# Kernel tuning notes

Hardware: AMD Instinct MI355X
Metric: run time of the kernel (lower is better)

## Reference

```python
import jax, jax.numpy as jnp
import numpy as np

DIM = 1024
INTER = 512
E = 32            # n_routed_experts
TOPK = 4          # n_activated_experts
GROUPS = 8        # n_expert_groups
TOPK_GROUPS = 4
SHARED_INTER = 2 * INTER  # n_shared_experts * moe_inter_dim
ROUTE_SCALE = 1.0
B, S = 8, 4096


def setup_inputs() -> dict:
    key = jax.random.key(0)
    ks = jax.random.split(key, 16)
    def xav(k, shape):
        fan_in, fan_out = shape[-2], shape[-1]
        lim = np.sqrt(6.0 / (fan_in + fan_out))
        return jax.random.uniform(k, shape, jnp.float32, -lim, lim)
    return {
        "x": jax.random.normal(ks[0], (B, S, DIM), jnp.float32),
        "gw": xav(ks[1], (DIM, E)),
        "gb": jnp.zeros((E,), jnp.float32),
        "w1": xav(ks[2], (E, DIM, INTER)),
        "b1": jnp.zeros((E, INTER), jnp.float32),
        "w3": xav(ks[3], (E, DIM, INTER)),
        "b3": jnp.zeros((E, INTER), jnp.float32),
        "w2": xav(ks[4], (E, INTER, DIM)),
        "b2": jnp.zeros((E, DIM), jnp.float32),
        "sw1": xav(ks[5], (DIM, SHARED_INTER)),
        "sb1": jnp.zeros((SHARED_INTER,), jnp.float32),
        "sw3": xav(ks[6], (DIM, SHARED_INTER)),
        "sb3": jnp.zeros((SHARED_INTER,), jnp.float32),
        "sw2": xav(ks[7], (SHARED_INTER, DIM)),
        "sb2": jnp.zeros((DIM,), jnp.float32),
    }


def _gate(xf, gw, gb):
    # scores: softmax over routed experts in fp32 (score_func='softmax')
    T = xf.shape[0]
    scores = jax.nn.softmax((xf @ gw + gb).astype(jnp.float32), axis=-1)  # [T, E]
    original_scores = scores
    # group-masked routing (n_expert_groups > 1)
    scores_g = scores.reshape(T, GROUPS, E // GROUPS)                     # [T, G, E/G]
    group_scores = jnp.sum(jax.lax.top_k(scores_g, 2)[0], axis=-1)        # [T, G]
    gidx = jax.lax.top_k(group_scores, TOPK_GROUPS)[1]                    # [T, topk_groups]
    keep = jnp.zeros((T, GROUPS), bool).at[jnp.arange(T)[:, None], gidx].set(True)
    masked = jnp.where(keep[:, :, None], scores_g, -jnp.inf).reshape(T, E)
    indices = jax.lax.top_k(masked, TOPK)[1]                              # [T, topk]
    weights = jnp.take_along_axis(original_scores, indices, axis=1) * ROUTE_SCALE
    return weights.astype(xf.dtype), indices


def reference(x, gw, gb, w1, b1, w3, b3, w2, b2, sw1, sb1, sw3, sb3, sw2, sb2):
    shape = x.shape
    xf = x.reshape(-1, DIM)                                               # [T, dim]
    T = xf.shape[0]
    weights, indices = _gate(xf, gw, gb)
    # dense combine weights [T, E]: w_e(t) = routing weight if expert e chosen for t else 0
    cw = jnp.zeros((T, E), xf.dtype).at[jnp.arange(T)[:, None], indices].add(weights)
    # scan over experts: y += w_e * SwiGLU_e(x). Zero weight -> zero contribution,
    # identical math to the masked dispatch/scatter-add in the torch code.
    def body(y, p):
        w1e, b1e, w3e, b3e, w2e, b2e, we = p
        h = jax.nn.silu(xf @ w1e + b1e) * (xf @ w3e + b3e)                # [T, inter]
        return y + we[:, None] * (h @ w2e + b2e), None
    y0 = jnp.zeros_like(xf)
    y, _ = jax.lax.scan(body, y0, (w1, b1, w3, b3, w2, b2, cw.T))
    # shared experts MLP (SwiGLU)
    z = (jax.nn.silu(xf @ sw1 + sb1) * (xf @ sw3 + sb3)) @ sw2 + sb2
    return (y + z).reshape(shape)
```

## Files before the change

kernel.cpp:

```cpp
#include <hip/hip_runtime.h>
#include <stdint.h>

#define DIM_    1024
#define INTER_  512

typedef short bf16x4 __attribute__((ext_vector_type(4)));
typedef short bf16x8 __attribute__((ext_vector_type(8)));
typedef float f32x4  __attribute__((ext_vector_type(4)));

__device__ __forceinline__ unsigned short f2bf(float f) {
  union { float f; unsigned u; } v; v.f = f;
  return (unsigned short)((v.u + 0x7FFFu + ((v.u >> 16) & 1u)) >> 16);
}
__device__ __forceinline__ unsigned f2bf2(float a, float b) {
  union { float f; unsigned u; } va, vb; va.f = a; vb.f = b;
  unsigned ra = (va.u + 0x7FFFu + ((va.u >> 16) & 1u)) >> 16;
  unsigned rb = (vb.u + 0x7FFFu + ((vb.u >> 16) & 1u)) >> 16;
  return ra | (rb << 16);
}
__device__ __forceinline__ float bfhi(unsigned u) {
  union { unsigned u; float f; } v; v.u = u & 0xffff0000u; return v.f;
}
__device__ __forceinline__ float bflo(unsigned u) {
  union { unsigned u; float f; } v; v.u = u << 16; return v.f;
}

__device__ __forceinline__ void gl16(const void* g, void* l) {
  __builtin_amdgcn_global_load_lds(
      (const __attribute__((address_space(1))) unsigned int*)g,
      (__attribute__((address_space(3))) unsigned int*)l, 16, 0, 0);
}

#define BARX() do { asm volatile("" ::: "memory"); \
                    __builtin_amdgcn_s_barrier();  \
                    asm volatile("" ::: "memory"); } while (0)

__global__ __launch_bounds__(256) void gate_kernel(
    const float* __restrict__ x, const float* __restrict__ gw,
    const float* __restrict__ gb, int* __restrict__ idx, float* __restrict__ wts,
    unsigned short* __restrict__ xb) {
  __shared__ double s_sc[4][32];
  __shared__ double s_gs[4][8];
  const int wid = threadIdx.x >> 6, lane = threadIdx.x & 63;
  const int t = blockIdx.x * 4 + wid;
  {
    const float* xrow = x + (size_t)t * DIM_ + lane * 16;
    unsigned short* xbrow = xb + (size_t)t * DIM_ + lane * 16;
    float4 f0 = *(const float4*)(xrow);
    float4 f1 = *(const float4*)(xrow + 4);
    float4 f2v = *(const float4*)(xrow + 8);
    float4 f3v = *(const float4*)(xrow + 12);
    uint4 o0, o1;
    o0.x = f2bf2(f0.x, f0.y);  o0.y = f2bf2(f0.z, f0.w);
    o0.z = f2bf2(f1.x, f1.y);  o0.w = f2bf2(f1.z, f1.w);
    o1.x = f2bf2(f2v.x, f2v.y); o1.y = f2bf2(f2v.z, f2v.w);
    o1.z = f2bf2(f3v.x, f3v.y); o1.w = f2bf2(f3v.z, f3v.w);
    *(uint4*)(xbrow) = o0;
    *(uint4*)(xbrow + 8) = o1;
  }
  const int e = lane & 31, half = lane >> 5;
  const float* xr  = x  + (size_t)t * DIM_ + half * 512;
  const float* gwp = gw + (size_t)half * 512 * 32 + e;
  double a0 = 0, a1 = 0, a2 = 0, a3 = 0;
  for (int k = 0; k < 512; k += 4) {
    float4 xv = *(const float4*)(xr + k);
    a0 += (double)xv.x * (double)gwp[(k + 0) * 32];
    a1 += (double)xv.y * (double)gwp[(k + 1) * 32];
    a2 += (double)xv.z * (double)gwp[(k + 2) * 32];
    a3 += (double)xv.w * (double)gwp[(k + 3) * 32];
  }
  double lg = (a0 + a1) + (a2 + a3);
  lg += __shfl_xor(lg, 32);
  lg += (double)gb[e];
  double m = lg;
  #pragma unroll
  for (int d = 1; d < 32; d <<= 1) m = fmax(m, __shfl_xor(m, d));
  double ex = exp(lg - m);
  double ssum = ex;
  #pragma unroll
  for (int d = 1; d < 32; d <<= 1) ssum += __shfl_xor(ssum, d);
  double sc = ex / ssum;
  double p  = __shfl_xor(sc, 1);
  double m1 = fmax(sc, p), n1 = fmin(sc, p);
  double m2 = __shfl_xor(m1, 2), n2 = __shfl_xor(n1, 2);
  double gs = (m1 >= m2) ? (m1 + fmax(n1, m2)) : (m2 + fmax(n2, m1));
  if (lane < 32) {
    s_sc[wid][e] = sc;
    if ((e & 3) == 0) s_gs[wid][e >> 2] = gs;
  }
  __syncthreads();
  if (lane == 0) {
    unsigned kmask = 0;
    for (int it = 0; it < 4; ++it) {
      int bg = 0; double bv = -1.0;
      for (int g = 0; g < 8; ++g)
        if (!((kmask >> g) & 1u) && s_gs[wid][g] > bv) { bv = s_gs[wid][g]; bg = g; }
      kmask |= 1u << bg;
    }
    unsigned umask = 0;
    for (int slot = 0; slot < 4; ++slot) {
      int be = 0; double bv = -1.0;
      for (int ee = 0; ee < 32; ++ee)
        if (((kmask >> (ee >> 2)) & 1u) && !((umask >> ee) & 1u) && s_sc[wid][ee] > bv) {
          bv = s_sc[wid][ee]; be = ee;
        }
      umask |= 1u << be;
      idx[t * 4 + slot] = be;
      wts[t * 4 + slot] = (float)bv;
    }
  }
}

__global__ __launch_bounds__(256) void count_kernel(const int* __restrict__ idx,
                                                    int* __restrict__ meta) {
  __shared__ int h[32];
  int tid = threadIdx.x;
  if (tid < 32) h[tid] = 0;
  __syncthreads();
  atomicAdd(&h[idx[blockIdx.x * 256 + tid]], 1);
  __syncthreads();
  if (tid < 32 && h[tid]) atomicAdd(&meta[tid], h[tid]);
}

__global__ void scan_kernel(int* __restrict__ meta) {
  int lane = threadIdx.x & 63;
  if (lane < 32) {
    int c = meta[lane];
    int pre = c;
    #pragma unroll
    for (int d = 1; d < 32; d <<= 1) { int t = __shfl_up(pre, d); if (lane >= d) pre += t; }
    int excl = pre - c;
    meta[64 + lane] = excl;
    meta[32 + lane] = excl;
    int nt = (c + 255) >> 8;
    int ntp = nt;
    #pragma unroll
    for (int d = 1; d < 32; d <<= 1) { int t = __shfl_up(ntp, d); if (lane >= d) ntp += t; }
    int ntExcl = ntp - nt;
    for (int k = 0; k < nt; ++k) { meta[128 + ntExcl + k] = lane; meta[1184 + ntExcl + k] = k << 8; }
    if (lane == 31) { meta[96] = excl + c; meta[97] = ntExcl + nt; }
  }
}

__global__ __launch_bounds__(256) void scatter_kernel(
    const int* __restrict__ idx, int* __restrict__ meta,
    int* __restrict__ tok, int* __restrict__ inv) {
  int i = blockIdx.x * 256 + threadIdx.x;
  int lane = threadIdx.x & 63;
  int e = idx[i];
  unsigned long long m = ~0ull;
  #pragma unroll
  for (int b = 0; b < 5; ++b) {
    unsigned long long vote = __ballot((e >> b) & 1);
    m &= ((e >> b) & 1) ? vote : ~vote;
  }
  int leader = __ffsll((long long)m) - 1;
  int rank = __popcll(m & ((1ull << lane) - 1));
  int base = 0;
  if (lane == leader) base = atomicAdd(&meta[32 + e], (int)__popcll(m));
  base = __shfl(base, leader);
  int p = base + rank;
  tok[p] = i >> 2;
  inv[i] = p;
}

__global__ __launch_bounds__(256) void repack_kernel(
    const float* __restrict__ src, unsigned short* __restrict__ dst,
    int K, int N, int tilesPerMat) {
  const int w = blockIdx.x * 4 + (threadIdx.x >> 6);
  const int j = threadIdx.x & 63;
  const int e = w / tilesPerMat, rem = w % tilesPerMat;
  const int kSteps = K >> 5;
  const int nt = rem / kSteps, kq = rem % kSteps;
  const float* s = src + (size_t)e * K * N + (size_t)(kq * 32) * N + nt * 64 + j;
  float v[32];
  #pragma unroll
  for (int kk = 0; kk < 32; ++kk) v[kk] = s[(size_t)kk * N];
  char* d = (char*)dst + (size_t)w * 4096 + j * 64;
  const int sz = (j & 3) ^ ((j >> 2) & 3);
  #pragma unroll
  for (int q = 0; q < 4; ++q) {
    int o = (q ^ sz) * 8;
    uint4 tv;
    tv.x = f2bf2(v[o + 0], v[o + 1]);
    tv.y = f2bf2(v[o + 2], v[o + 3]);
    tv.z = f2bf2(v[o + 4], v[o + 5]);
    tv.w = f2bf2(v[o + 6], v[o + 7]);
    *(uint4*)(d + q * 16) = tv;
  }
}

__global__ __launch_bounds__(256) void repack13_kernel(
    const float* __restrict__ src1, const float* __restrict__ src3,
    unsigned short* __restrict__ dst, int K, int N, int jtTiles) {
  const int w = blockIdx.x * 4 + (threadIdx.x >> 6);
  const int j = threadIdx.x & 63;
  const int kSteps = K >> 5;
  const int tpm = jtTiles * kSteps;
  const int e = w / tpm, rem = w % tpm;
  const int jt = rem / kSteps, kq = rem % kSteps;
  const int jg = jt * 64 + j;
  const int c = ((jg >> 5) << 4) + (jg & 15);
  const float* s = (((jg >> 4) & 1) ? src3 : src1)
                 + (size_t)e * K * N + (size_t)(kq * 32) * N + c;
  float v[32];
  #pragma unroll
  for (int kk = 0; kk < 32; ++kk) v[kk] = s[(size_t)kk * N];
  char* d = (char*)dst + (size_t)w * 4096 + j * 64;
  const int sz = (j & 3) ^ ((j >> 2) & 3);
  #pragma unroll
  for (int q = 0; q < 4; ++q) {
    int o = (q ^ sz) * 8;
    uint4 tv;
    tv.x = f2bf2(v[o + 0], v[o + 1]);
    tv.y = f2bf2(v[o + 2], v[o + 3]);
    tv.z = f2bf2(v[o + 4], v[o + 5]);
    tv.w = f2bf2(v[o + 6], v[o + 7]);
    *(uint4*)(d + q * 16) = tv;
  }
}


#define G8_PRE()                                                              \
  const int tid = threadIdx.x, lane = tid & 63, wave = tid >> 6;              \
  const int wm = wave >> 2, wn = wave & 3;                                    \
  const int f = lane & 15, g = lane >> 4;                                     \
  const int wud = wave >> 2, wlo = wave & 3;                                  \
  const int row_in = wlo * 16 + (lane >> 2);                                  \
  const int szr = (row_in & 3) ^ ((row_in >> 2) & 3);                         \
  const int qs = (((lane & 3) ^ szr) << 4);                                   \
  const int btile_off = wlo * 1024 + lane * 16;                               \
  const int wv1k = wave * 1024;                                               \
  const int awb = wm * 8192;                                                  \
  const int wn4 = wn * 4096;                                                  \
  int aoff[4];                                                                \
  _Pragma("unroll")                                                           \
  for (int ii = 0; ii < 4; ++ii) {                                            \
    int u16 = ii * 16 + f;                                                    \
    aoff[ii] = u16 * 64 + ((g ^ ((u16 & 3) ^ ((u16 >> 2) & 3))) << 4);        \
  }                                                                           \
  f32x4 acc[8][4];                                                            \
  const f32x4 zz = {0.f, 0.f, 0.f, 0.f};                                      \
  _Pragma("unroll")                                                           \
  for (int mi = 0; mi < 8; ++mi)                                              \
    _Pragma("unroll")                                                         \
    for (int ni = 0; ni < 4; ++ni) acc[mi][ni] = zz;

#define G8_PH(p, UMAXv)                                                       \
  {                                                                           \
    const char* sb_ = lds + ((p) >> 1) * 32768;                               \
    const char* ab_ = sb_ + awb + ((p) & 1) * 4096;                           \
    const char* bb_ = sb_ + 16384 + wn4;                                      \
    bf16x8 af_[4], bv_[4];                                                    \
    _Pragma("unroll")                                                         \
    for (int mi = 0; mi < 4; ++mi) af_[mi] = *(const bf16x8*)(ab_ + aoff[mi]);\
    _Pragma("unroll")                                                         \
    for (int ni = 0; ni < 4; ++ni) bv_[ni] = *(const bf16x8*)(bb_ + aoff[ni]);\
    int u_ = I4 + 3 + ((p) >> 1);                                             \
    if (u_ >= (UMAXv)) u_ = (UMAXv) - 1;                                      \
    char* td_ = lds + (((((p) >> 1) + 3) & 3) * 32768);                       \
    if ((p) & 1) {                                                            \
      gl16(pB0 + (size_t)u_ * 4096, td_ + 16384 + wv1k);                      \
      gl16(pB1 + (size_t)u_ * 4096, td_ + 24576 + wv1k);                      \
    } else {                                                                  \
      gl16(pA0 + u_ * 64, td_ + wv1k);                                        \
      gl16(pA1 + u_ * 64, td_ + 8192 + wv1k);                                 \
    }                                                                         \
    BARX();                                                                   \
    __builtin_amdgcn_s_setprio(1);                                            \
    _Pragma("unroll")                                                         \
    for (int ni = 0; ni < 4; ++ni)                                            \
      _Pragma("unroll")                                                       \
      for (int mi = 0; mi < 4; ++mi)                                          \
        acc[((p) & 1) * 4 + mi][ni] = __builtin_amdgcn_mfma_f32_16x16x32_bf16(\
            af_[mi], bv_[ni], acc[((p) & 1) * 4 + mi][ni], 0, 0, 0);          \
    __builtin_amdgcn_s_setprio(0);                                            \
    if ((p) & 1) asm volatile("s_waitcnt vmcnt(8)" ::: "memory");             \
    BARX();                                                                   \
  }

#define G8_BODY(UMAXv)                                                        \
  _Pragma("unroll")                                                           \
  for (int uu = 0; uu < 3; ++uu) {                                            \
    gl16(pA0 + uu * 64, lds + uu * 32768 + wv1k);                             \
    gl16(pA1 + uu * 64, lds + uu * 32768 + 8192 + wv1k);                      \
    gl16(pB0 + (size_t)uu * 4096, lds + uu * 32768 + 16384 + wv1k);           \
    gl16(pB1 + (size_t)uu * 4096, lds + uu * 32768 + 24576 + wv1k);           \
  }                                                                           \
  asm volatile("s_waitcnt vmcnt(8)" ::: "memory");                            \
  BARX();                                                                     \
  for (int I = 0; I < (UMAXv) / 4; ++I) {                                     \
    const int I4 = I * 4;                                                     \
    G8_PH(0, UMAXv); G8_PH(1, UMAXv); G8_PH(2, UMAXv); G8_PH(3, UMAXv);       \
    G8_PH(4, UMAXv); G8_PH(5, UMAXv); G8_PH(6, UMAXv); G8_PH(7, UMAXv);       \
  }

__global__ __launch_bounds__(512, 2) void s1_kernel(
    const unsigned short* __restrict__ xb, const unsigned short* __restrict__ w13,
    const float* __restrict__ sb1, const float* __restrict__ sb3,
    unsigned short* __restrict__ Hs) {
  __shared__ char lds[131072];
  const int m0 = blockIdx.y * 256;
  G8_PRE();
  const char* pA0 = (const char*)xb + (size_t)(m0 + wud * 64 + row_in) * 2048 + qs;
  const char* pA1 = pA0 + (size_t)128 * 2048;
  const char* pB0 = (const char*)w13 + ((size_t)(blockIdx.x * 4 + wud) * 32) * 4096 + btile_off;
  const char* pB1 = (const char*)w13 + ((size_t)(blockIdx.x * 4 + 2 + wud) * 32) * 4096 + btile_off;
  G8_BODY(32);
  const int colb = blockIdx.x * 128;
  #pragma unroll
  for (int p2 = 0; p2 < 2; ++p2) {
    int c = colb + wn * 32 + p2 * 16 + f;
    float bb1 = sb1[c], bb3 = sb3[c];
    #pragma unroll
    for (int m8 = 0; m8 < 8; ++m8) {
      int row = m0 + wm * 128 + (m8 >> 2) * 64 + (m8 & 3) * 16 + g * 4;
      #pragma unroll
      for (int r = 0; r < 4; ++r) {
        float v1 = acc[m8][2 * p2][r] + bb1;
        float v3 = acc[m8][2 * p2 + 1][r] + bb3;
        float h = (v1 / (1.f + __expf(-v1))) * v3;
        Hs[(size_t)(row + r) * 1024 + c] = f2bf(h);
      }
    }
  }
}

__global__ __launch_bounds__(512, 2) void s2_kernel(
    const unsigned short* __restrict__ Hs, const unsigned short* __restrict__ b2i,
    const float* __restrict__ sb2, float* __restrict__ out) {
  __shared__ char lds[131072];
  const int m0 = blockIdx.y * 256;
  G8_PRE();
  const char* pA0 = (const char*)Hs + (size_t)(m0 + wud * 64 + row_in) * 2048 + qs;
  const char* pA1 = pA0 + (size_t)128 * 2048;
  const char* pB0 = (const char*)b2i + ((size_t)(blockIdx.x * 4 + wud) * 32) * 4096 + btile_off;
  const char* pB1 = (const char*)b2i + ((size_t)(blockIdx.x * 4 + 2 + wud) * 32) * 4096 + btile_off;
  G8_BODY(32);
  #pragma unroll
  for (int ni = 0; ni < 4; ++ni) {
    int c = blockIdx.x * 256 + wn * 64 + ni * 16 + f;
    float bb = sb2[c];
    #pragma unroll
    for (int m8 = 0; m8 < 8; ++m8) {
      int row = m0 + wm * 128 + (m8 >> 2) * 64 + (m8 & 3) * 16 + g * 4;
      #pragma unroll
      for (int r = 0; r < 4; ++r)
        out[(size_t)(row + r) * 1024 + c] = acc[m8][ni][r] + bb;
    }
  }
}

__global__ __launch_bounds__(512, 2) void g1_kernel(
    const unsigned short* __restrict__ xb, const unsigned short* __restrict__ w13,
    const float* __restrict__ b1, const float* __restrict__ b3,
    const int* __restrict__ tok, const int* __restrict__ meta,
    unsigned short* __restrict__ H) {
  __shared__ char lds[131072];
  if ((int)blockIdx.y >= meta[97]) return;
  const int e = meta[128 + blockIdx.y], m0 = meta[1184 + blockIdx.y];
  const int off_e = meta[64 + e], nrem = meta[e] - m0;
  G8_PRE();
  const int r0a = wud * 64 + row_in;
  const int ix0 = off_e + m0 + ((r0a < nrem) ? r0a : 0);
  const int ix1 = off_e + m0 + ((r0a + 128 < nrem) ? r0a + 128 : 0);
  const char* pA0 = (const char*)xb + (size_t)tok[ix0] * 2048 + qs;
  const char* pA1 = (const char*)xb + (size_t)tok[ix1] * 2048 + qs;
  const char* pB0 = (const char*)w13 + ((size_t)(e * 16 + blockIdx.x * 4 + wud) * 32) * 4096 + btile_off;
  const char* pB1 = (const char*)w13 + ((size_t)(e * 16 + blockIdx.x * 4 + 2 + wud) * 32) * 4096 + btile_off;
  G8_BODY(32);
  const int colb = blockIdx.x * 128;
  #pragma unroll
  for (int p2 = 0; p2 < 2; ++p2) {
    int c = colb + wn * 32 + p2 * 16 + f;
    float bb1 = b1[e * 512 + c], bb3 = b3[e * 512 + c];
    #pragma unroll
    for (int m8 = 0; m8 < 8; ++m8) {
      int row = wm * 128 + (m8 >> 2) * 64 + (m8 & 3) * 16 + g * 4;
      #pragma unroll
      for (int r = 0; r < 4; ++r) {
        if (row + r < nrem) {
          float v1 = acc[m8][2 * p2][r] + bb1;
          float v3 = acc[m8][2 * p2 + 1][r] + bb3;
          float h = (v1 / (1.f + __expf(-v1))) * v3;
          H[(size_t)(off_e + m0 + row + r) * 512 + c] = f2bf(h);
        }
      }
    }
  }
}

__global__ __launch_bounds__(512, 2) void g2_kernel(
    const unsigned short* __restrict__ H, const unsigned short* __restrict__ w2i,
    const float* __restrict__ b2, const int* __restrict__ meta,
    unsigned short* __restrict__ Y, int cbase) {
  __shared__ char lds[131072];
  if ((int)blockIdx.y >= meta[97]) return;
  const int e = meta[128 + blockIdx.y], m0 = meta[1184 + blockIdx.y];
  const int off_e = meta[64 + e], nrem = meta[e] - m0;
  G8_PRE();
  const int r0a = wud * 64 + row_in;
  const int ix0 = off_e + m0 + ((r0a < nrem) ? r0a : 0);
  const int ix1 = off_e + m0 + ((r0a + 128 < nrem) ? r0a + 128 : 0);
  const char* pA0 = (const char*)H + (size_t)ix0 * 1024 + qs;
  const char* pA1 = (const char*)H + (size_t)ix1 * 1024 + qs;
  const int nt0 = (cbase >> 6) + blockIdx.x * 4;
  const char* pB0 = (const char*)w2i + ((size_t)(e * 16 + nt0 + wud) * 16) * 4096 + btile_off;
  const char* pB1 = (const char*)w2i + ((size_t)(e * 16 + nt0 + 2 + wud) * 16) * 4096 + btile_off;
  G8_BODY(16);
  #pragma unroll
  for (int ni = 0; ni < 4; ++ni) {
    int ycol = blockIdx.x * 256 + wn * 64 + ni * 16 + f;
    float bb = b2[e * 1024 + cbase + ycol];
    #pragma unroll
    for (int m8 = 0; m8 < 8; ++m8) {
      int row = wm * 128 + (m8 >> 2) * 64 + (m8 & 3) * 16 + g * 4;
      #pragma unroll
      for (int r = 0; r < 4; ++r) {
        if (row + r < nrem)
          Y[(size_t)(off_e + m0 + row + r) * 512 + ycol] = f2bf(acc[m8][ni][r] + bb);
      }
    }
  }
}

__global__ __launch_bounds__(256) void combine_kernel(
    const unsigned short* __restrict__ Y, const int* __restrict__ inv,
    const float* __restrict__ wts, float* __restrict__ out, int cbase) {
  int t = blockIdx.x * 2 + (threadIdx.x >> 7);
  int c = (threadIdx.x & 127) * 4;
  int4 iv = *(const int4*)(inv + t * 4);
  float4 wv = *(const float4*)(wts + t * 4);
  float* op = out + (size_t)t * 1024 + cbase + c;
  float4 o = *(float4*)op;
  uint2 u;
  u = *(const uint2*)(Y + (size_t)iv.x * 512 + c);
  o.x += wv.x * bflo(u.x); o.y += wv.x * bfhi(u.x);
  o.z += wv.x * bflo(u.y); o.w += wv.x * bfhi(u.y);
  u = *(const uint2*)(Y + (size_t)iv.y * 512 + c);
  o.x += wv.y * bflo(u.x); o.y += wv.y * bfhi(u.x);
  o.z += wv.y * bflo(u.y); o.w += wv.y * bfhi(u.y);
  u = *(const uint2*)(Y + (size_t)iv.z * 512 + c);
  o.x += wv.z * bflo(u.x); o.y += wv.z * bfhi(u.x);
  o.z += wv.z * bflo(u.y); o.w += wv.z * bfhi(u.y);
  u = *(const uint2*)(Y + (size_t)iv.w * 512 + c);
  o.x += wv.w * bflo(u.x); o.y += wv.w * bfhi(u.x);
  o.z += wv.w * bflo(u.y); o.w += wv.w * bfhi(u.y);
  *(float4*)op = o;
}

extern "C" void kernel_launch(void* const* d_in, const int* in_sizes, int n_in,
                              void* d_out, int out_size, void* d_ws, size_t ws_size,
                              hipStream_t stream) {
  const float* x   = (const float*)d_in[0];
  const float* gw  = (const float*)d_in[1];
  const float* gb  = (const float*)d_in[2];
  const float* w1  = (const float*)d_in[3];
  const float* b1  = (const float*)d_in[4];
  const float* w3  = (const float*)d_in[5];
  const float* b3  = (const float*)d_in[6];
  const float* w2  = (const float*)d_in[7];
  const float* b2  = (const float*)d_in[8];
  const float* sw1 = (const float*)d_in[9];
  const float* sb1 = (const float*)d_in[10];
  const float* sw3 = (const float*)d_in[11];
  const float* sb3 = (const float*)d_in[12];
  const float* sw2 = (const float*)d_in[13];
  const float* sb2 = (const float*)d_in[14];
  float* out = (float*)d_out;
  char* ws = (char*)d_ws;

  const size_t OFF_XB   = 134217728;
  const size_t OFF_W13I = 201326592;
  const size_t OFF_W2I  = 268435456;
  const size_t OFF_S13I = 301989888;
  const size_t OFF_SW2I = 306184192;
  const size_t OFF_IDX  = 308281344;
  const size_t OFF_WTS  = 308805632;
  const size_t OFF_TOK  = 309329920;
  const size_t OFF_INV  = 309854208;
  const size_t OFF_META = 310378496;
  if (ws_size < OFF_META + 8960) return;

  unsigned short* H    = (unsigned short*)ws;
  unsigned short* xb   = (unsigned short*)(ws + OFF_XB);
  unsigned short* Yb   = (unsigned short*)(ws + OFF_XB);
  unsigned short* w13i = (unsigned short*)(ws + OFF_W13I);
  unsigned short* w2i  = (unsigned short*)(ws + OFF_W2I);
  unsigned short* s13i = (unsigned short*)(ws + OFF_S13I);
  unsigned short* sw2i = (unsigned short*)(ws + OFF_SW2I);
  int*   idx  = (int*)(ws + OFF_IDX);
  float* wts  = (float*)(ws + OFF_WTS);
  int*   tokl = (int*)(ws + OFF_TOK);
  int*   inv  = (int*)(ws + OFF_INV);
  int*   meta = (int*)(ws + OFF_META);

  hipMemsetAsync(meta, 0, 128, stream);
  gate_kernel<<<dim3(8192), dim3(256), 0, stream>>>(x, gw, gb, idx, wts, xb);
  count_kernel<<<dim3(512), dim3(256), 0, stream>>>(idx, meta);
  scan_kernel<<<dim3(1), dim3(64), 0, stream>>>(meta);
  scatter_kernel<<<dim3(512), dim3(256), 0, stream>>>(idx, meta, tokl, inv);
  repack13_kernel<<<dim3(4096), dim3(256), 0, stream>>>(w1, w3, w13i, 1024, 512, 16);
  repack_kernel<<<dim3(2048), dim3(256), 0, stream>>>(w2, w2i, 512, 1024, 256);
  repack13_kernel<<<dim3(256), dim3(256), 0, stream>>>(sw1, sw3, s13i, 1024, 1024, 32);
  repack_kernel<<<dim3(128), dim3(256), 0, stream>>>(sw2, sw2i, 1024, 1024, 512);
  s1_kernel<<<dim3(8, 128), dim3(512), 0, stream>>>(xb, s13i, sb1, sb3, H);
  s2_kernel<<<dim3(4, 128), dim3(512), 0, stream>>>(H, sw2i, sb2, out);
  g1_kernel<<<dim3(4, 544), dim3(512), 0, stream>>>(xb, w13i, b1, b3, tokl, meta, H);
  g2_kernel<<<dim3(2, 544), dim3(512), 0, stream>>>(H, w2i, b2, meta, Yb, 0);
  combine_kernel<<<dim3(16384), dim3(256), 0, stream>>>(Yb, inv, wts, out, 0);
  g2_kernel<<<dim3(2, 544), dim3(512), 0, stream>>>(H, w2i, b2, meta, Yb, 512);
  combine_kernel<<<dim3(16384), dim3(256), 0, stream>>>(Yb, inv, wts, out, 512);
}
```

Before: 1.641 ms.

## Swizzle GEMM block order across XCDs and reuse B fragments across phases

Flattens the 2D grids of the four grouped/shared GEMM kernels into 1D and remaps block ids so consecutive logical tiles land on the same XCD. The goal is to improve L2 reuse of the shared A/B tiles. It also loads the B LDS fragments only on even phases and keeps them in registers for the following odd phase, cutting redundant LDS reads. This adds register pressure, and the swizzle assumes the block count divides evenly by 8.

```diff
diff --git a/kernel.cpp b/kernel.cpp
--- a/kernel.cpp
+++ b/kernel.cpp
@@ -239,6 +239,7 @@
     int u16 = ii * 16 + f;                                                    \
     aoff[ii] = u16 * 64 + ((g ^ ((u16 & 3) ^ ((u16 >> 2) & 3))) << 4);        \
   }                                                                           \
+  bf16x8 bvp[4];                                                              \
   f32x4 acc[8][4];                                                            \
   const f32x4 zz = {0.f, 0.f, 0.f, 0.f};                                      \
   _Pragma("unroll")                                                           \
@@ -250,12 +251,15 @@
   {                                                                           \
     const char* sb_ = lds + ((p) >> 1) * 32768;                               \
     const char* ab_ = sb_ + awb + ((p) & 1) * 4096;                           \
-    const char* bb_ = sb_ + 16384 + wn4;                                      \
-    bf16x8 af_[4], bv_[4];                                                    \
+    bf16x8 af_[4];                                                            \
     _Pragma("unroll")                                                         \
     for (int mi = 0; mi < 4; ++mi) af_[mi] = *(const bf16x8*)(ab_ + aoff[mi]);\
-    _Pragma("unroll")                                                         \
-    for (int ni = 0; ni < 4; ++ni) bv_[ni] = *(const bf16x8*)(bb_ + aoff[ni]);\
+    if (!((p) & 1)) {                                                         \
+      const char* bb_ = sb_ + 16384 + wn4;                                    \
+      _Pragma("unroll")                                                       \
+      for (int ni = 0; ni < 4; ++ni)                                          \
+        bvp[ni] = *(const bf16x8*)(bb_ + aoff[ni]);                           \
+    }                                                                         \
     int u_ = I4 + 3 + ((p) >> 1);                                             \
     if (u_ >= (UMAXv)) u_ = (UMAXv) - 1;                                      \
     char* td_ = lds + (((((p) >> 1) + 3) & 3) * 32768);                       \
@@ -273,7 +277,7 @@
       _Pragma("unroll")                                                       \
       for (int mi = 0; mi < 4; ++mi)                                          \
         acc[((p) & 1) * 4 + mi][ni] = __builtin_amdgcn_mfma_f32_16x16x32_bf16(\
-            af_[mi], bv_[ni], acc[((p) & 1) * 4 + mi][ni], 0, 0, 0);          \
+            af_[mi], bvp[ni], acc[((p) & 1) * 4 + mi][ni], 0, 0, 0);          \
     __builtin_amdgcn_s_setprio(0);                                            \
     if ((p) & 1) asm volatile("s_waitcnt vmcnt(8)" ::: "memory");             \
     BARX();                                                                   \
@@ -295,19 +299,27 @@
     G8_PH(4, UMAXv); G8_PH(5, UMAXv); G8_PH(6, UMAXv); G8_PH(7, UMAXv);       \
   }
 
+#define XCD_SWZ(GXv)                                                          \
+  const int nb_ = gridDim.x;                                                  \
+  const int b_ = blockIdx.x;                                                  \
+  const int w_ = (b_ & 7) * (nb_ >> 3) + (b_ >> 3);                           \
+  const int bx = w_ % (GXv);                                                  \
+  const int by = w_ / (GXv);
+
 __global__ __launch_bounds__(512, 2) void s1_kernel(
     const unsigned short* __restrict__ xb, const unsigned short* __restrict__ w13,
     const float* __restrict__ sb1, const float* __restrict__ sb3,
     unsigned short* __restrict__ Hs) {
   __shared__ char lds[131072];
-  const int m0 = blockIdx.y * 256;
+  XCD_SWZ(8);
+  const int m0 = by * 256;
   G8_PRE();
   const char* pA0 = (const char*)xb + (size_t)(m0 + wud * 64 + row_in) * 2048 + qs;
   const char* pA1 = pA0 + (size_t)128 * 2048;
-  const char* pB0 = (const char*)w13 + ((size_t)(blockIdx.x * 4 + wud) * 32) * 4096 + btile_off;
-  const char* pB1 = (const char*)w13 + ((size_t)(blockIdx.x * 4 + 2 + wud) * 32) * 4096 + btile_off;
+  const char* pB0 = (const char*)w13 + ((size_t)(bx * 4 + wud) * 32) * 4096 + btile_off;
+  const char* pB1 = (const char*)w13 + ((size_t)(bx * 4 + 2 + wud) * 32) * 4096 + btile_off;
   G8_BODY(32);
-  const int colb = blockIdx.x * 128;
+  const int colb = bx * 128;
   #pragma unroll
   for (int p2 = 0; p2 < 2; ++p2) {
     int c = colb + wn * 32 + p2 * 16 + f;
@@ -330,16 +342,17 @@
     const unsigned short* __restrict__ Hs, const unsigned short* __restrict__ b2i,
     const float* __restrict__ sb2, float* __restrict__ out) {
   __shared__ char lds[131072];
-  const int m0 = blockIdx.y * 256;
+  XCD_SWZ(4);
+  const int m0 = by * 256;
   G8_PRE();
   const char* pA0 = (const char*)Hs + (size_t)(m0 + wud * 64 + row_in) * 2048 + qs;
   const char* pA1 = pA0 + (size_t)128 * 2048;
-  const char* pB0 = (const char*)b2i + ((size_t)(blockIdx.x * 4 + wud) * 32) * 4096 + btile_off;
-  const char* pB1 = (const char*)b2i + ((size_t)(blockIdx.x * 4 + 2 + wud) * 32) * 4096 + btile_off;
+  const char* pB0 = (const char*)b2i + ((size_t)(bx * 4 + wud) * 32) * 4096 + btile_off;
+  const char* pB1 = (const char*)b2i + ((size_t)(bx * 4 + 2 + wud) * 32) * 4096 + btile_off;
   G8_BODY(32);
   #pragma unroll
   for (int ni = 0; ni < 4; ++ni) {
-    int c = blockIdx.x * 256 + wn * 64 + ni * 16 + f;
+    int c = bx * 256 + wn * 64 + ni * 16 + f;
     float bb = sb2[c];
     #pragma unroll
     for (int m8 = 0; m8 < 8; ++m8) {
@@ -357,8 +370,9 @@
     const int* __restrict__ tok, const int* __restrict__ meta,
     unsigned short* __restrict__ H) {
   __shared__ char lds[131072];
-  if ((int)blockIdx.y >= meta[97]) return;
-  const int e = meta[128 + blockIdx.y], m0 = meta[1184 + blockIdx.y];
+  XCD_SWZ(4);
+  if (by >= meta[97]) return;
+  const int e = meta[128 + by], m0 = meta[1184 + by];
   const int off_e = meta[64 + e], nrem = meta[e] - m0;
   G8_PRE();
   const int r0a = wud * 64 + row_in;
@@ -366,10 +380,10 @@
   const int ix1 = off_e + m0 + ((r0a + 128 < nrem) ? r0a + 128 : 0);
   const char* pA0 = (const char*)xb + (size_t)tok[ix0] * 2048 + qs;
   const char* pA1 = (const char*)xb + (size_t)tok[ix1] * 2048 + qs;
-  const char* pB0 = (const char*)w13 + ((size_t)(e * 16 + blockIdx.x * 4 + wud) * 32) * 4096 + btile_off;
-  const char* pB1 = (const char*)w13 + ((size_t)(e * 16 + blockIdx.x * 4 + 2 + wud) * 32) * 4096 + btile_off;
+  const char* pB0 = (const char*)w13 + ((size_t)(e * 16 + bx * 4 + wud) * 32) * 4096 + btile_off;
+  const char* pB1 = (const char*)w13 + ((size_t)(e * 16 + bx * 4 + 2 + wud) * 32) * 4096 + btile_off;
   G8_BODY(32);
-  const int colb = blockIdx.x * 128;
+  const int colb = bx * 128;
   #pragma unroll
   for (int p2 = 0; p2 < 2; ++p2) {
     int c = colb + wn * 32 + p2 * 16 + f;
@@ -395,8 +409,9 @@
     const float* __restrict__ b2, const int* __restrict__ meta,
     unsigned short* __restrict__ Y, int cbase) {
   __shared__ char lds[131072];
-  if ((int)blockIdx.y >= meta[97]) return;
-  const int e = meta[128 + blockIdx.y], m0 = meta[1184 + blockIdx.y];
+  XCD_SWZ(2);
+  if (by >= meta[97]) return;
+  const int e = meta[128 + by], m0 = meta[1184 + by];
   const int off_e = meta[64 + e], nrem = meta[e] - m0;
   G8_PRE();
   const int r0a = wud * 64 + row_in;
@@ -404,13 +419,13 @@
   const int ix1 = off_e + m0 + ((r0a + 128 < nrem) ? r0a + 128 : 0);
   const char* pA0 = (const char*)H + (size_t)ix0 * 1024 + qs;
   const char* pA1 = (const char*)H + (size_t)ix1 * 1024 + qs;
-  const int nt0 = (cbase >> 6) + blockIdx.x * 4;
+  const int nt0 = (cbase >> 6) + bx * 4;
   const char* pB0 = (const char*)w2i + ((size_t)(e * 16 + nt0 + wud) * 16) * 4096 + btile_off;
   const char* pB1 = (const char*)w2i + ((size_t)(e * 16 + nt0 + 2 + wud) * 16) * 4096 + btile_off;
   G8_BODY(16);
   #pragma unroll
   for (int ni = 0; ni < 4; ++ni) {
-    int ycol = blockIdx.x * 256 + wn * 64 + ni * 16 + f;
+    int ycol = bx * 256 + wn * 64 + ni * 16 + f;
     float bb = b2[e * 1024 + cbase + ycol];
     #pragma unroll
     for (int m8 = 0; m8 < 8; ++m8) {
@@ -504,11 +519,11 @@
   repack_kernel<<<dim3(2048), dim3(256), 0, stream>>>(w2, w2i, 512, 1024, 256);
   repack13_kernel<<<dim3(256), dim3(256), 0, stream>>>(sw1, sw3, s13i, 1024, 1024, 32);
   repack_kernel<<<dim3(128), dim3(256), 0, stream>>>(sw2, sw2i, 1024, 1024, 512);
-  s1_kernel<<<dim3(8, 128), dim3(512), 0, stream>>>(xb, s13i, sb1, sb3, H);
-  s2_kernel<<<dim3(4, 128), dim3(512), 0, stream>>>(H, sw2i, sb2, out);
-  g1_kernel<<<dim3(4, 544), dim3(512), 0, stream>>>(xb, w13i, b1, b3, tokl, meta, H);
-  g2_kernel<<<dim3(2, 544), dim3(512), 0, stream>>>(H, w2i, b2, meta, Yb, 0);
+  s1_kernel<<<dim3(1024), dim3(512), 0, stream>>>(xb, s13i, sb1, sb3, H);
+  s2_kernel<<<dim3(512), dim3(512), 0, stream>>>(H, sw2i, sb2, out);
+  g1_kernel<<<dim3(2176), dim3(512), 0, stream>>>(xb, w13i, b1, b3, tokl, meta, H);
+  g2_kernel<<<dim3(1088), dim3(512), 0, stream>>>(H, w2i, b2, meta, Yb, 0);
   combine_kernel<<<dim3(16384), dim3(256), 0, stream>>>(Yb, inv, wts, out, 0);
-  g2_kernel<<<dim3(2, 544), dim3(512), 0, stream>>>(H, w2i, b2, meta, Yb, 512);
+  g2_kernel<<<dim3(1088), dim3(512), 0, stream>>>(H, w2i, b2, meta, Yb, 512);
   combine_kernel<<<dim3(16384), dim3(256), 0, stream>>>(Yb, inv, wts, out, 512);
 }
```

Result: faster. 1.592 ms (-3.0%).
